# Optimization experiments

Measured on AMD Instinct MI355X. Metric: run time of the kernel, lower is better.

Reference implementation:

```python
import jax, jax.numpy as jnp
import numpy as np

N = 30000
F_IN = 500
HID = 16
OUT = 3
E = 960000


def setup_inputs() -> dict:
    key = jax.random.key(0)
    ks = jax.random.split(key, 10)
    x = jax.random.normal(ks[0], (N, F_IN), dtype=jnp.float32)
    edge_index = jax.random.randint(ks[1], (2, E), 0, N, dtype=jnp.int32)
    # CNN params (torch Conv1d: weight [out, in, k], bias [out])
    s1 = 1.0 / np.sqrt(1 * 3)
    s2 = 1.0 / np.sqrt(HID * 3)
    conv1_w = jax.random.uniform(ks[2], (HID, 1, 3), jnp.float32, -s1, s1)
    conv1_b = jax.random.uniform(ks[3], (HID,), jnp.float32, -s1, s1)
    conv2_w = jax.random.uniform(ks[4], (HID, HID, 3), jnp.float32, -s2, s2)
    conv2_b = jax.random.uniform(ks[5], (HID,), jnp.float32, -s2, s2)
    # GCNConv params (glorot weight [in, out], zero bias)
    g1 = np.sqrt(6.0 / (HID + HID))
    g2 = np.sqrt(6.0 / (HID + OUT))
    gcn1_w = jax.random.uniform(ks[6], (HID, HID), jnp.float32, -g1, g1)
    gcn1_b = jnp.zeros((HID,), jnp.float32)
    gcn2_w = jax.random.uniform(ks[7], (HID, OUT), jnp.float32, -g2, g2)
    gcn2_b = jnp.zeros((OUT,), jnp.float32)
    return {"x": x, "conv1_w": conv1_w, "conv1_b": conv1_b,
            "conv2_w": conv2_w, "conv2_b": conv2_b,
            "gcn1_w": gcn1_w, "gcn1_b": gcn1_b,
            "gcn2_w": gcn2_w, "gcn2_b": gcn2_b,
            "edge_index": edge_index}


def _conv1d(x, w, b):
    # x: [N, C_in, L], w: [C_out, C_in, 3], padding=1
    y = jax.lax.conv_general_dilated(
        x, w, window_strides=(1,), padding=[(1, 1)],
        dimension_numbers=("NCH", "OIH", "NCH"))
    return y + b[None, :, None]


def _gcn_conv(x, w, b, src, dst, n):
    # x: [n, d_in] -> [n, d_out]; Kipf normalization with self-loops
    h = x @ w
    loop = jnp.arange(n, dtype=src.dtype)
    s = jnp.concatenate([src, loop])
    d = jnp.concatenate([dst, loop])
    deg = jax.ops.segment_sum(jnp.ones_like(d, dtype=h.dtype), d, num_segments=n)
    dinv = jnp.where(deg > 0, jax.lax.rsqrt(deg), 0.0)
    norm = dinv[s] * dinv[d]                      # [E+n]
    msg = h[s] * norm[:, None]                    # gather + scale
    return jax.ops.segment_sum(msg, d, num_segments=n) + b


def reference(x, conv1_w, conv1_b, conv2_w, conv2_b,
              gcn1_w, gcn1_b, gcn2_w, gcn2_b, edge_index):
    # CNN feature extractor over feature axis
    h = x[:, None, :]                             # [N, 1, F_IN]
    h = jax.nn.relu(_conv1d(h, conv1_w, conv1_b))  # [N, HID, F_IN]
    h = jax.nn.relu(_conv1d(h, conv2_w, conv2_b))  # [N, HID, F_IN]
    h = jnp.max(h, axis=2)                        # global max pool -> [N, HID]
    # GCN
    src, dst = edge_index[0], edge_index[1]
    n = h.shape[0]
    h = jax.nn.relu(_gcn_conv(h, gcn1_w, gcn1_b, src, dst, n))
    h = _gcn_conv(h, gcn2_w, gcn2_b, src, dst, n)  # [N, OUT]
    return jax.nn.log_softmax(h, axis=1)
```

## Files before the change

### kernel.cpp

```cpp
#include <hip/hip_runtime.h>
#include <hip/hip_bf16.h>

#define N_NODES 30000
#define F_INLEN 500
#define HID 16
#define OUTC 3
#define NEDGE 960000
#define YP 16
#define NBIN 938
#define HBLK 128
#define EPRH (NEDGE / HBLK)
#define ECAP 1536

typedef float  f32x4 __attribute__((ext_vector_type(4)));
typedef float  f32x2 __attribute__((ext_vector_type(2)));
typedef short  s16x8 __attribute__((ext_vector_type(8)));

static __device__ __forceinline__ unsigned short f2bf(float f) {
    unsigned int u = __float_as_uint(f);
    unsigned int r = (u + 0x7fffu + ((u >> 16) & 1u)) >> 16;
    return (unsigned short)r;
}
static __device__ __forceinline__ unsigned int pack_bf16x2(float v0, float v1) {
#if __has_builtin(__builtin_amdgcn_cvt_pk_bf16_f32)
    typedef __bf16 bf16x2_t __attribute__((ext_vector_type(2)));
    union { bf16x2_t v; unsigned int u; } cv;
    cv.v = __builtin_amdgcn_cvt_pk_bf16_f32(v0, v1);
    return cv.u;
#else
    return __builtin_amdgcn_perm(__float_as_uint(v1), __float_as_uint(v0), 0x07060302);
#endif
}

__global__ __launch_bounds__(256) void hist_kernel(
    const float* __restrict__ w2, short* __restrict__ bfragsG,
    const int* __restrict__ dst, int* __restrict__ degi, int* __restrict__ cntbase)
{
    const int tid = threadIdx.x;
    if (blockIdx.x == HBLK) {
        if (tid < 64) {
            const int n16 = tid & 15, q = tid >> 4;
#pragma unroll
            for (int j = 0; j < 8; j++) {
                {
                    const int c = q * 8 + j;
                    const int t = c >> 4, i = c & 15;
                    bfragsG[tid * 16 + j] = (short)f2bf(w2[n16 * 48 + i * 3 + t]);
                }
                {
                    const int c = 32 + q * 8 + j;
                    short v = 0;
                    if (c < 48) { const int t = c >> 4, i = c & 15; v = (short)f2bf(w2[n16 * 48 + i * 3 + t]); }
                    bfragsG[tid * 16 + 8 + j] = v;
                }
            }
        }
        return;
    }
    __shared__ int histH[NBIN];
    for (int i = tid; i < NBIN; i += 256) histH[i] = 0;
    __syncthreads();
    const int e0 = blockIdx.x * EPRH;
    for (int e = e0 + tid; e < e0 + EPRH; e += 256) {
        const int d = dst[e];
        atomicAdd(&histH[d >> 5], 1);
        atomicAdd(&degi[d], 1);
    }
    __syncthreads();
    for (int i = tid; i < NBIN; i += 256) cntbase[blockIdx.x * NBIN + i] = histH[i];
}

__global__ __launch_bounds__(256, 8) void conv_reorder(
    const float* __restrict__ x,
    const float* __restrict__ w1, const float* __restrict__ b1,
    const float* __restrict__ b2, const short* __restrict__ bfragsG,
    const int* __restrict__ src, const int* __restrict__ dst,
    const int* __restrict__ degi, const int* __restrict__ cntbase,
    int* __restrict__ packed, int* __restrict__ binstart,
    float* __restrict__ h0)
{
    __shared__ __align__(16) unsigned short yh[516 * YP];
    __shared__ float red[64];

    const int tid = threadIdx.x;

    if (blockIdx.x < HBLK) {
        int* scA    = (int*)yh;
        int* scB    = scA + NBIN;
        int* totb   = scB + NBIN;
        int* cursor = totb + NBIN;
        const int blk = blockIdx.x;
        for (int bin = tid; bin < NBIN; bin += 256) {
            int tot = 0, psum = 0;
            for (int k = 0; k < HBLK; k++) {
                const int c = cntbase[k * NBIN + bin];
                tot += c;
                if (k < blk) psum += c;
            }
            scA[bin]    = tot;
            totb[bin]   = tot;
            cursor[bin] = psum;
        }
        __syncthreads();
        int* pA = scA; int* pB = scB;
        for (int off = 1; off < NBIN; off <<= 1) {
            for (int i = tid; i < NBIN; i += 256)
                pB[i] = pA[i] + ((i >= off) ? pA[i - off] : 0);
            __syncthreads();
            int* tp = pA; pA = pB; pB = tp;
        }
        for (int i = tid; i < NBIN; i += 256) {
            const int excl = pA[i] - totb[i];
            cursor[i] += excl;
            if (blk == 0) binstart[i] = excl;
        }
        if (blk == 0 && tid == 0) binstart[NBIN] = NEDGE;
        __syncthreads();
        const int e0 = blk * EPRH;
        for (int e = e0 + tid; e < e0 + EPRH; e += 256) {
            const int d = dst[e];
            const int pos = atomicAdd(&cursor[d >> 5], 1);
            packed[pos] = src[e] | (d << 15);
        }
        return;
    }

    const int node = blockIdx.x - HBLK;
    const int dgi  = degi[node];
    const int lane = tid & 63;
    const int wave = tid >> 6;
    const int n16  = lane & 15;
    const int q    = lane >> 4;

    {
        const int ri = tid >> 4;
        const int row = (ri == 0) ? 0 : (500 + ri);
        yh[row * YP + (tid & 15)] = 0;
    }
    const s16x8* bfp = (const s16x8*)(bfragsG + lane * 16);
    const s16x8 bh0 = bfp[0], bh1 = bfp[1];

    f32x2 wt0[8], wt1[8], wt2[8], bbv[8];
#pragma unroll
    for (int cp = 0; cp < 8; cp++) {
        const int c0 = 2 * cp, c1 = 2 * cp + 1;
        wt0[cp] = (f32x2){w1[c0 * 3 + 0], w1[c1 * 3 + 0]};
        wt1[cp] = (f32x2){w1[c0 * 3 + 1], w1[c1 * 3 + 1]};
        wt2[cp] = (f32x2){w1[c0 * 3 + 2], w1[c1 * 3 + 2]};
        bbv[cp] = (f32x2){b1[c0], b1[c1]};
    }

    const float* xr = x + (long long)node * F_INLEN;
    for (int p = tid; p < 500; p += 256) {
        const float xm = (p > 0)   ? xr[p - 1] : 0.f;
        const float x0 = xr[p];
        const float xq = (p < 499) ? xr[p + 1] : 0.f;
        const f32x2 xv0 = {xm, xm}, xv1 = {x0, x0}, xv2 = {xq, xq};
        const f32x2 zero = {0.f, 0.f};
        unsigned int hp[8];
#pragma unroll
        for (int cp = 0; cp < 8; cp++) {
            f32x2 a = __builtin_elementwise_fma(wt0[cp], xv0, bbv[cp]);
            a = __builtin_elementwise_fma(wt1[cp], xv1, a);
            a = __builtin_elementwise_fma(wt2[cp], xv2, a);
            a = __builtin_elementwise_max(a, zero);
            hp[cp] = pack_bf16x2(a[0], a[1]);
        }
        uint4* d = (uint4*)&yh[(p + 1) * YP];
        d[0] = make_uint4(hp[0], hp[1], hp[2], hp[3]);
        d[1] = make_uint4(hp[4], hp[5], hp[6], hp[7]);
    }
    __syncthreads();

    const unsigned short* ybase = yh + (n16 + (q >> 1)) * YP + (q & 1) * 8
                                     + wave * (8 * 16 * YP);
    f32x4 mxv = {-3.0e38f, -3.0e38f, -3.0e38f, -3.0e38f};
    f32x4 mxt = {-3.0e38f, -3.0e38f, -3.0e38f, -3.0e38f};
#pragma unroll
    for (int it = 0; it < 8; it++) {
        const s16x8 ah0 = *(const s16x8*)(ybase + it * (16 * YP));
        const s16x8 ah1 = *(const s16x8*)(ybase + it * (16 * YP) + 2 * YP);
        f32x4 acc = {0.f, 0.f, 0.f, 0.f};
        acc = __builtin_amdgcn_mfma_f32_16x16x32_bf16(ah0, bh0, acc, 0, 0, 0);
        acc = __builtin_amdgcn_mfma_f32_16x16x32_bf16(ah1, bh1, acc, 0, 0, 0);
        if (it < 7) mxv = __builtin_elementwise_max(mxv, acc);
        else        mxt = __builtin_elementwise_max(mxt, acc);
    }
    if (wave < 3 || q == 0) mxv = __builtin_elementwise_max(mxv, mxt);
    float m = fmaxf(fmaxf(mxv[0], mxv[1]), fmaxf(mxv[2], mxv[3]));
    m = fmaxf(m, __shfl_xor(m, 16));
    m = fmaxf(m, __shfl_xor(m, 32));
    if (lane < 16) red[wave * 16 + lane] = m;
    __syncthreads();
    if (tid < 16) {
        const float mm = fmaxf(fmaxf(red[tid], red[16 + tid]), fmaxf(red[32 + tid], red[48 + tid]));
        const float dv = rsqrtf((float)(dgi + 1));
        h0[node * HID + tid] = fmaxf(mm + b2[tid], 0.f) * dv;
    }
}

__global__ __launch_bounds__(512) void agg1_kernel(
    const int* __restrict__ binstart, int* __restrict__ packed,
    const float* __restrict__ h0,
    const float* __restrict__ W1, const float* __restrict__ b1g,
    const float* __restrict__ W2, float4* __restrict__ t2p4,
    int* __restrict__ binofs)
{
    __shared__ float w1s[256];
    __shared__ float w2s[48];
    __shared__ float b1s[16];
    __shared__ float accS[32 * 17];
    __shared__ int eL[ECAP];
    __shared__ int srt[ECAP];
    __shared__ int h32[32], ls32[32], lofs32[32];
    const int tid = threadIdx.x;
    const int blk = blockIdx.x;
    if (tid < 256) w1s[tid] = W1[tid];
    if (tid < 48) w2s[tid] = W2[tid];
    if (tid < 16) b1s[tid] = b1g[tid];
    if (tid < 32) h32[tid] = 0;
    const int beg = binstart[blk];
    const int cnt = binstart[blk + 1] - beg;
    __syncthreads();
    for (int j = tid; j < cnt; j += 512) {
        const int p = packed[beg + j];
        eL[j] = p;
        atomicAdd(&h32[(p >> 15) & 31], 1);
    }
    __syncthreads();
    if (tid < 32) {
        const int v = h32[tid];
        int inc = v;
#pragma unroll
        for (int off = 1; off < 32; off <<= 1) {
            const int y = __shfl_up(inc, off);
            if (tid >= off) inc += y;
        }
        ls32[tid] = inc - v;
        lofs32[tid] = inc - v;
    }
    __syncthreads();
    for (int j = tid; j < cnt; j += 512) {
        const int p = eL[j];
        const int pos = atomicAdd(&lofs32[(p >> 15) & 31], 1);
        srt[pos] = p;
    }
    __syncthreads();
    for (int j = tid; j < cnt; j += 512) packed[beg + j] = srt[j];
    if (tid < 32) {
        binofs[blk * 64 + tid]      = ls32[tid];
        binofs[blk * 64 + 32 + tid] = h32[tid];
    }
    const int n = tid >> 4;
    const int eslot = (tid >> 2) & 3;
    const int q = tid & 3;
    const int node = blk * 32 + n;
    const bool valid = node < N_NODES;
    f32x4 acc = {0.f, 0.f, 0.f, 0.f};
    if (valid) {
        const int s0 = ls32[n];
        const int s1 = s0 + h32[n];
        for (int i = s0 + eslot; i < s1; i += 4) {
            const int s = srt[i] & 32767;
            acc += *(const f32x4*)(h0 + s * HID + q * 4);
        }
    }
#pragma unroll
    for (int c = 0; c < 4; c++) {
        acc[c] += __shfl_xor(acc[c], 4);
        acc[c] += __shfl_xor(acc[c], 8);
    }
    if (valid && eslot == 0) {
        acc += *(const f32x4*)(h0 + node * HID + q * 4);
        accS[n * 17 + q * 4 + 0] = acc[0];
        accS[n * 17 + q * 4 + 1] = acc[1];
        accS[n * 17 + q * 4 + 2] = acc[2];
        accS[n * 17 + q * 4 + 3] = acc[3];
    }
    __syncthreads();
    if (tid < 128) {
        const int n2 = tid >> 2;
        const int node2 = blk * 32 + n2;
        if (node2 < N_NODES) {
            const float dv = rsqrtf((float)(h32[n2] + 1));
            const int q2 = tid & 3;
            float y0 = 0.f, y1 = 0.f, y2 = 0.f, y3 = 0.f;
#pragma unroll
            for (int i = 0; i < 16; i++) {
                const float a = accS[n2 * 17 + i];
                y0 = fmaf(a, w1s[i * 16 + q2 * 4 + 0], y0);
                y1 = fmaf(a, w1s[i * 16 + q2 * 4 + 1], y1);
                y2 = fmaf(a, w1s[i * 16 + q2 * 4 + 2], y2);
                y3 = fmaf(a, w1s[i * 16 + q2 * 4 + 3], y3);
            }
            float d0 = 0.f, d1 = 0.f, d2 = 0.f;
            const float yv[4] = {y0, y1, y2, y3};
#pragma unroll
            for (int j = 0; j < 4; j++) {
                const int o = q2 * 4 + j;
                const float h = fmaxf(b1s[o] + dv * yv[j], 0.f);
                d0 = fmaf(h, w2s[o * 3 + 0], d0);
                d1 = fmaf(h, w2s[o * 3 + 1], d1);
                d2 = fmaf(h, w2s[o * 3 + 2], d2);
            }
            d0 += __shfl_xor(d0, 1); d0 += __shfl_xor(d0, 2);
            d1 += __shfl_xor(d1, 1); d1 += __shfl_xor(d1, 2);
            d2 += __shfl_xor(d2, 1); d2 += __shfl_xor(d2, 2);
            if (q2 == 0) t2p4[node2] = make_float4(d0 * dv, d1 * dv, d2 * dv, dv);
        }
    }
}

__global__ __launch_bounds__(512) void agg2_kernel(
    const int* __restrict__ binstart, const int* __restrict__ packed,
    const float4* __restrict__ t2p4, const int* __restrict__ binofs,
    const float* __restrict__ b2g, float* __restrict__ out)
{
    __shared__ int eL[ECAP];
    __shared__ int ofs[64];
    const int tid = threadIdx.x;
    const int blk = blockIdx.x;
    const int beg = binstart[blk];
    const int cnt = binstart[blk + 1] - beg;
    if (tid < 64) ofs[tid] = binofs[blk * 64 + tid];
    for (int j = tid; j < cnt; j += 512) eL[j] = packed[beg + j];
    __syncthreads();
    const int n = tid >> 4;
    const int ln16 = tid & 15;
    const int node = blk * 32 + n;
    float a0 = 0.f, a1 = 0.f, a2 = 0.f;
    if (node < N_NODES) {
        const int s0 = ofs[n];
        const int s1 = s0 + ofs[32 + n];
        for (int i = s0 + ln16; i < s1; i += 16) {
            const int s = eL[i] & 32767;
            const float4 v = t2p4[s];
            a0 += v.x; a1 += v.y; a2 += v.z;
        }
    }
#pragma unroll
    for (int msk = 1; msk < 16; msk <<= 1) {
        a0 += __shfl_xor(a0, msk);
        a1 += __shfl_xor(a1, msk);
        a2 += __shfl_xor(a2, msk);
    }
    if (ln16 == 0 && node < N_NODES) {
        const float4 self = t2p4[node];
        const float dv = self.w;
        const float z0 = b2g[0] + dv * (a0 + self.x);
        const float z1 = b2g[1] + dv * (a1 + self.y);
        const float z2 = b2g[2] + dv * (a2 + self.z);
        const float m = fmaxf(z0, fmaxf(z1, z2));
        const float lg = m + logf(expf(z0 - m) + expf(z1 - m) + expf(z2 - m));
        out[node * 3 + 0] = z0 - lg;
        out[node * 3 + 1] = z1 - lg;
        out[node * 3 + 2] = z2 - lg;
    }
}

extern "C" void kernel_launch(void* const* d_in, const int* in_sizes, int n_in,
                              void* d_out, int out_size, void* d_ws, size_t ws_size,
                              hipStream_t stream)
{
    const float* x   = (const float*)d_in[0];
    const float* w1  = (const float*)d_in[1];
    const float* b1  = (const float*)d_in[2];
    const float* w2  = (const float*)d_in[3];
    const float* b2  = (const float*)d_in[4];
    const float* g1w = (const float*)d_in[5];
    const float* g1b = (const float*)d_in[6];
    const float* g2w = (const float*)d_in[7];
    const float* g2b = (const float*)d_in[8];
    const int*   ei  = (const int*)d_in[9];
    const int* src = ei;
    const int* dst = ei + NEDGE;

    float* ws = (float*)d_ws;
    float*  h0      = ws;
    float4* t2p4    = (float4*)(ws + 480000);
    int*    degi    = (int*)(ws + 600000);
    int*    cntbase = (int*)(ws + 630000);
    int*    binstart= (int*)(ws + 750064);
    int*    packed  = (int*)(ws + 751104);
    int*    binofs  = (int*)(ws + 1711104);
    short*  bfragsG = (short*)(ws + 1771136);
    float*  out     = (float*)d_out;

    hipMemsetAsync(degi, 0, N_NODES * sizeof(int), stream);
    hist_kernel<<<HBLK + 1, 256, 0, stream>>>(w2, bfragsG, dst, degi, cntbase);
    conv_reorder<<<HBLK + N_NODES, 256, 0, stream>>>(x, w1, b1, b2, bfragsG,
                                                     src, dst, degi, cntbase,
                                                     packed, binstart, h0);
    agg1_kernel<<<NBIN, 512, 0, stream>>>(binstart, packed, h0,
                                          g1w, g1b, g2w, t2p4, binofs);
    agg2_kernel<<<NBIN, 512, 0, stream>>>(binstart, packed, t2p4, binofs, g2b, out);
}
```

Before: 216.6 us.

## Replace binned counting sort with per-node CSR built via global scan

The two-level bin histogram plus local in-block resort of edges is replaced by a per-node CSR. Degrees are counted with global atomics, a single-block scan kernel computes node offsets, and the reorder blocks scatter source ids directly through per-node atomic cursors. Both aggregation kernels then read edge ranges straight from global memory instead of staging and resorting bins in shared memory. This removes the per-bin prefix computation and shared-memory resort, but adds a serial single-block scan launch and more contended global atomics on per-node cursors.

```diff
diff --git a/kernel.cpp b/kernel.cpp
--- a/kernel.cpp
+++ b/kernel.cpp
@@ -10,7 +10,6 @@
 #define NBIN 938
 #define HBLK 128
 #define EPRH (NEDGE / HBLK)
-#define ECAP 1536
 
 typedef float  f32x4 __attribute__((ext_vector_type(4)));
 typedef float  f32x2 __attribute__((ext_vector_type(2)));
@@ -34,7 +33,7 @@
 
 __global__ __launch_bounds__(256) void hist_kernel(
     const float* __restrict__ w2, short* __restrict__ bfragsG,
-    const int* __restrict__ dst, int* __restrict__ degi, int* __restrict__ cntbase)
+    const int* __restrict__ dst, int* __restrict__ degi)
 {
     const int tid = threadIdx.x;
     if (blockIdx.x == HBLK) {
@@ -57,17 +56,37 @@
         }
         return;
     }
-    __shared__ int histH[NBIN];
-    for (int i = tid; i < NBIN; i += 256) histH[i] = 0;
-    __syncthreads();
     const int e0 = blockIdx.x * EPRH;
     for (int e = e0 + tid; e < e0 + EPRH; e += 256) {
-        const int d = dst[e];
-        atomicAdd(&histH[d >> 5], 1);
-        atomicAdd(&degi[d], 1);
-    }
+        atomicAdd(&degi[dst[e]], 1);
+    }
+}
+
+__global__ __launch_bounds__(1024) void scan_kernel(
+    const int* __restrict__ degi, int* __restrict__ nodestart,
+    int* __restrict__ nodecur)
+{
+    __shared__ int ts[1024];
+    const int t = threadIdx.x;
+    const int c0 = t * 30;
+    const int c1 = (c0 + 30 < N_NODES) ? c0 + 30 : N_NODES;
+    int s = 0;
+    for (int j = c0; j < c1; ++j) s += degi[j];
+    ts[t] = s;
     __syncthreads();
-    for (int i = tid; i < NBIN; i += 256) cntbase[blockIdx.x * NBIN + i] = histH[i];
+    for (int off = 1; off < 1024; off <<= 1) {
+        const int add = (t >= off) ? ts[t - off] : 0;
+        __syncthreads();
+        ts[t] += add;
+        __syncthreads();
+    }
+    int run = (t > 0) ? ts[t - 1] : 0;
+    for (int j = c0; j < c1; ++j) {
+        nodestart[j] = run;
+        nodecur[j]   = run;
+        run += degi[j];
+    }
+    if (t == 1023) nodestart[N_NODES] = run;
 }
 
 __global__ __launch_bounds__(256, 8) void conv_reorder(
@@ -75,9 +94,8 @@
     const float* __restrict__ w1, const float* __restrict__ b1,
     const float* __restrict__ b2, const short* __restrict__ bfragsG,
     const int* __restrict__ src, const int* __restrict__ dst,
-    const int* __restrict__ degi, const int* __restrict__ cntbase,
-    int* __restrict__ packed, int* __restrict__ binstart,
-    float* __restrict__ h0)
+    const int* __restrict__ degi, int* __restrict__ nodecur,
+    int* __restrict__ packed, float* __restrict__ h0)
 {
     __shared__ __align__(16) unsigned short yh[516 * YP];
     __shared__ float red[64];
@@ -85,42 +103,11 @@
     const int tid = threadIdx.x;
 
     if (blockIdx.x < HBLK) {
-        int* scA    = (int*)yh;
-        int* scB    = scA + NBIN;
-        int* totb   = scB + NBIN;
-        int* cursor = totb + NBIN;
-        const int blk = blockIdx.x;
-        for (int bin = tid; bin < NBIN; bin += 256) {
-            int tot = 0, psum = 0;
-            for (int k = 0; k < HBLK; k++) {
-                const int c = cntbase[k * NBIN + bin];
-                tot += c;
-                if (k < blk) psum += c;
-            }
-            scA[bin]    = tot;
-            totb[bin]   = tot;
-            cursor[bin] = psum;
-        }
-        __syncthreads();
-        int* pA = scA; int* pB = scB;
-        for (int off = 1; off < NBIN; off <<= 1) {
-            for (int i = tid; i < NBIN; i += 256)
-                pB[i] = pA[i] + ((i >= off) ? pA[i - off] : 0);
-            __syncthreads();
-            int* tp = pA; pA = pB; pB = tp;
-        }
-        for (int i = tid; i < NBIN; i += 256) {
-            const int excl = pA[i] - totb[i];
-            cursor[i] += excl;
-            if (blk == 0) binstart[i] = excl;
-        }
-        if (blk == 0 && tid == 0) binstart[NBIN] = NEDGE;
-        __syncthreads();
-        const int e0 = blk * EPRH;
+        const int e0 = blockIdx.x * EPRH;
         for (int e = e0 + tid; e < e0 + EPRH; e += 256) {
             const int d = dst[e];
-            const int pos = atomicAdd(&cursor[d >> 5], 1);
-            packed[pos] = src[e] | (d << 15);
+            const int pos = atomicAdd(&nodecur[d], 1);
+            packed[pos] = src[e];
         }
         return;
     }
@@ -200,70 +187,33 @@
 }
 
 __global__ __launch_bounds__(512) void agg1_kernel(
-    const int* __restrict__ binstart, int* __restrict__ packed,
+    const int* __restrict__ nodestart, const int* __restrict__ packed,
     const float* __restrict__ h0,
     const float* __restrict__ W1, const float* __restrict__ b1g,
-    const float* __restrict__ W2, float4* __restrict__ t2p4,
-    int* __restrict__ binofs)
+    const float* __restrict__ W2, float4* __restrict__ t2p4)
 {
     __shared__ float w1s[256];
     __shared__ float w2s[48];
     __shared__ float b1s[16];
     __shared__ float accS[32 * 17];
-    __shared__ int eL[ECAP];
-    __shared__ int srt[ECAP];
-    __shared__ int h32[32], ls32[32], lofs32[32];
+    __shared__ int degL[32];
     const int tid = threadIdx.x;
     const int blk = blockIdx.x;
     if (tid < 256) w1s[tid] = W1[tid];
     if (tid < 48) w2s[tid] = W2[tid];
     if (tid < 16) b1s[tid] = b1g[tid];
-    if (tid < 32) h32[tid] = 0;
-    const int beg = binstart[blk];
-    const int cnt = binstart[blk + 1] - beg;
-    __syncthreads();
-    for (int j = tid; j < cnt; j += 512) {
-        const int p = packed[beg + j];
-        eL[j] = p;
-        atomicAdd(&h32[(p >> 15) & 31], 1);
-    }
-    __syncthreads();
-    if (tid < 32) {
-        const int v = h32[tid];
-        int inc = v;
-#pragma unroll
-        for (int off = 1; off < 32; off <<= 1) {
-            const int y = __shfl_up(inc, off);
-            if (tid >= off) inc += y;
-        }
-        ls32[tid] = inc - v;
-        lofs32[tid] = inc - v;
-    }
-    __syncthreads();
-    for (int j = tid; j < cnt; j += 512) {
-        const int p = eL[j];
-        const int pos = atomicAdd(&lofs32[(p >> 15) & 31], 1);
-        srt[pos] = p;
-    }
-    __syncthreads();
-    for (int j = tid; j < cnt; j += 512) packed[beg + j] = srt[j];
-    if (tid < 32) {
-        binofs[blk * 64 + tid]      = ls32[tid];
-        binofs[blk * 64 + 32 + tid] = h32[tid];
-    }
+
     const int n = tid >> 4;
     const int eslot = (tid >> 2) & 3;
     const int q = tid & 3;
     const int node = blk * 32 + n;
     const bool valid = node < N_NODES;
+    int s0 = 0, s1 = 0;
+    if (valid) { s0 = nodestart[node]; s1 = nodestart[node + 1]; }
     f32x4 acc = {0.f, 0.f, 0.f, 0.f};
-    if (valid) {
-        const int s0 = ls32[n];
-        const int s1 = s0 + h32[n];
-        for (int i = s0 + eslot; i < s1; i += 4) {
-            const int s = srt[i] & 32767;
-            acc += *(const f32x4*)(h0 + s * HID + q * 4);
-        }
+    for (int i = s0 + eslot; i < s1; i += 4) {
+        const int s = packed[i];
+        acc += *(const f32x4*)(h0 + s * HID + q * 4);
     }
 #pragma unroll
     for (int c = 0; c < 4; c++) {
@@ -276,13 +226,14 @@
         accS[n * 17 + q * 4 + 1] = acc[1];
         accS[n * 17 + q * 4 + 2] = acc[2];
         accS[n * 17 + q * 4 + 3] = acc[3];
+        if (q == 0) degL[n] = s1 - s0;
     }
     __syncthreads();
     if (tid < 128) {
         const int n2 = tid >> 2;
         const int node2 = blk * 32 + n2;
         if (node2 < N_NODES) {
-            const float dv = rsqrtf((float)(h32[n2] + 1));
+            const float dv = rsqrtf((float)(degL[n2] + 1));
             const int q2 = tid & 3;
             float y0 = 0.f, y1 = 0.f, y2 = 0.f, y3 = 0.f;
 #pragma unroll
@@ -312,31 +263,22 @@
 }
 
 __global__ __launch_bounds__(512) void agg2_kernel(
-    const int* __restrict__ binstart, const int* __restrict__ packed,
-    const float4* __restrict__ t2p4, const int* __restrict__ binofs,
-    const float* __restrict__ b2g, float* __restrict__ out)
-{
-    __shared__ int eL[ECAP];
-    __shared__ int ofs[64];
+    const int* __restrict__ nodestart, const int* __restrict__ packed,
+    const float4* __restrict__ t2p4, const float* __restrict__ b2g,
+    float* __restrict__ out)
+{
     const int tid = threadIdx.x;
     const int blk = blockIdx.x;
-    const int beg = binstart[blk];
-    const int cnt = binstart[blk + 1] - beg;
-    if (tid < 64) ofs[tid] = binofs[blk * 64 + tid];
-    for (int j = tid; j < cnt; j += 512) eL[j] = packed[beg + j];
-    __syncthreads();
     const int n = tid >> 4;
     const int ln16 = tid & 15;
     const int node = blk * 32 + n;
     float a0 = 0.f, a1 = 0.f, a2 = 0.f;
-    if (node < N_NODES) {
-        const int s0 = ofs[n];
-        const int s1 = s0 + ofs[32 + n];
-        for (int i = s0 + ln16; i < s1; i += 16) {
-            const int s = eL[i] & 32767;
-            const float4 v = t2p4[s];
-            a0 += v.x; a1 += v.y; a2 += v.z;
-        }
+    int s0 = 0, s1 = 0;
+    if (node < N_NODES) { s0 = nodestart[node]; s1 = nodestart[node + 1]; }
+    for (int i = s0 + ln16; i < s1; i += 16) {
+        const int s = packed[i];
+        const float4 v = t2p4[s];
+        a0 += v.x; a1 += v.y; a2 += v.z;
     }
 #pragma unroll
     for (int msk = 1; msk < 16; msk <<= 1) {
@@ -376,22 +318,22 @@
     const int* dst = ei + NEDGE;
 
     float* ws = (float*)d_ws;
-    float*  h0      = ws;
-    float4* t2p4    = (float4*)(ws + 480000);
-    int*    degi    = (int*)(ws + 600000);
-    int*    cntbase = (int*)(ws + 630000);
-    int*    binstart= (int*)(ws + 750064);
-    int*    packed  = (int*)(ws + 751104);
-    int*    binofs  = (int*)(ws + 1711104);
-    short*  bfragsG = (short*)(ws + 1771136);
-    float*  out     = (float*)d_out;
+    float*  h0       = ws;
+    float4* t2p4     = (float4*)(ws + 480000);
+    int*    degi     = (int*)(ws + 600000);
+    int*    nodestart= (int*)(ws + 630000);
+    int*    nodecur  = (int*)(ws + 660016);
+    int*    packed   = (int*)(ws + 690016);
+    short*  bfragsG  = (short*)(ws + 1650016);
+    float*  out      = (float*)d_out;
 
     hipMemsetAsync(degi, 0, N_NODES * sizeof(int), stream);
-    hist_kernel<<<HBLK + 1, 256, 0, stream>>>(w2, bfragsG, dst, degi, cntbase);
+    hist_kernel<<<HBLK + 1, 256, 0, stream>>>(w2, bfragsG, dst, degi);
+    scan_kernel<<<1, 1024, 0, stream>>>(degi, nodestart, nodecur);
     conv_reorder<<<HBLK + N_NODES, 256, 0, stream>>>(x, w1, b1, b2, bfragsG,
-                                                     src, dst, degi, cntbase,
-                                                     packed, binstart, h0);
-    agg1_kernel<<<NBIN, 512, 0, stream>>>(binstart, packed, h0,
-                                          g1w, g1b, g2w, t2p4, binofs);
-    agg2_kernel<<<NBIN, 512, 0, stream>>>(binstart, packed, t2p4, binofs, g2b, out);
-}
+                                                     src, dst, degi, nodecur,
+                                                     packed, h0);
+    agg1_kernel<<<NBIN, 512, 0, stream>>>(nodestart, packed, h0,
+                                          g1w, g1b, g2w, t2p4);
+    agg2_kernel<<<NBIN, 512, 0, stream>>>(nodestart, packed, t2p4, g2b, out);
+}
```

Result: slower. 283.6 us (+31.0%).
